# Kernel tuning notes

Hardware: AMD Instinct MI355X
Metric: run time of the kernel (lower is better)

Reference implementation:

```python
import jax, jax.numpy as jnp
import numpy as np
from jax.scipy.special import logsumexp

EXPERT_NUM = 64
MOE_TOPK = 2

def setup_inputs() -> dict:
    key = jax.random.key(0)
    k1, k2 = jax.random.split(key)
    x = jax.random.normal(k1, (4, 4096, 4096), dtype=jnp.float32)
    # nn.Linear(input_size, expert_num).weight has shape [expert_num, input_size]
    W = jax.random.normal(k2, (EXPERT_NUM, 4096), dtype=jnp.float32) * (1.0 / np.sqrt(4096))
    return {"x": x, "W": W}

def reference(x, W):
    # logits: [B, S, E]
    logits = jnp.einsum('bsd,ed->bse', x, W)
    k = min(MOE_TOPK + 1, EXPERT_NUM)  # torch takes topk+1 then slices
    topk_logits, topk_indices = jax.lax.top_k(logits, k)
    topk_logits = topk_logits[..., :MOE_TOPK]     # [B, S, K]
    topk_indices = topk_indices[..., :MOE_TOPK]   # [B, S, K]
    # regularized=True: softmax over the top-k logits in float32
    topk_scores = jax.nn.softmax(topk_logits.astype(jnp.float32), axis=-1).astype(logits.dtype)
    # scatter into zeros; topk indices are unique so one-hot sum == scatter-set
    scores_filtered = jnp.sum(
        jax.nn.one_hot(topk_indices, EXPERT_NUM, dtype=logits.dtype) * topk_scores[..., None],
        axis=-2)  # [B, S, E]
    # router_z loss, per-token [B, S]
    log_z = logsumexp(logits, axis=-1)
    loss = log_z ** 2
    return logits, scores_filtered, loss
```

## Files before the change

kernel.cpp:

```cpp
#include <hip/hip_runtime.h>
#include <math.h>

#define TTOK 16384
#define DD   4096
#define EE   64
#define TM   64
#define BK   64
#define KSL  4
#define KW   (DD / KSL)
#define NCHB (KW / BK)

typedef __attribute__((ext_vector_type(8))) short short8;
typedef __attribute__((ext_vector_type(4))) float f32x4;

static __device__ __forceinline__ unsigned short f2bf(float f) {
    unsigned u = __float_as_uint(f);
    u += 0x7FFFu + ((u >> 16) & 1u);
    return (unsigned short)(u >> 16);
}
static __device__ __forceinline__ float bf2f(unsigned short h) {
    return __uint_as_float(((unsigned)h) << 16);
}
static __device__ __forceinline__ void cvt8(float4 a, float4 b, short8& hi, short8& lo) {
    const float v[8] = {a.x, a.y, a.z, a.w, b.x, b.y, b.z, b.w};
#pragma unroll
    for (int j = 0; j < 8; ++j) {
        const unsigned short h = f2bf(v[j]);
        hi[j] = (short)h;
        lo[j] = (short)f2bf(v[j] - bf2f(h));
    }
}

__global__ void w_convert(const float* __restrict__ W,
                          unsigned short* __restrict__ whi,
                          unsigned short* __restrict__ wlo) {
    const int i = (blockIdx.x * blockDim.x + threadIdx.x) * 4;
    if (i >= EE * DD) return;
    const float4 v = *reinterpret_cast<const float4*>(W + i);
    ushort4 h, l;
    h.x = f2bf(v.x); l.x = f2bf(v.x - bf2f(h.x));
    h.y = f2bf(v.y); l.y = f2bf(v.y - bf2f(h.y));
    h.z = f2bf(v.z); l.z = f2bf(v.z - bf2f(h.z));
    h.w = f2bf(v.w); l.w = f2bf(v.w - bf2f(h.w));
    *reinterpret_cast<ushort4*>(whi + i) = h;
    *reinterpret_cast<ushort4*>(wlo + i) = l;
}

__global__ __launch_bounds__(256, 4)
void gemm_part(const float* __restrict__ x,
               const unsigned short* __restrict__ whi,
               const unsigned short* __restrict__ wlo,
               float* __restrict__ part)
{
    __shared__ unsigned short xh[TM * 64];
    __shared__ unsigned short xl[TM * 64];
    __shared__ unsigned short whs[TM * 64];
    __shared__ unsigned short wls[TM * 64];

    const int tid  = threadIdx.x;
    const int wv   = tid >> 6;
    const int lane = tid & 63;
    const int m    = lane & 15;
    const int q    = lane >> 4;
    const int tile = blockIdx.x & 255;
    const int ks   = blockIdx.x >> 8;
    const int t0   = tile * TM;
    const int k0   = ks * KW;

    const int sr = tid >> 3;
    const int sj = tid & 7;
    const int sp = (sj ^ (sr & 7)) * 8;

    const float* gx0          = x   + (size_t)(t0 + sr) * DD + k0 + sj * 8;
    const float* gx1          = gx0 + (size_t)32 * DD;
    const unsigned short* gh0 = whi + (size_t)sr * DD + k0 + sj * 8;
    const unsigned short* gh1 = gh0 + (size_t)32 * DD;
    const unsigned short* gl0 = wlo + (size_t)sr * DD + k0 + sj * 8;
    const unsigned short* gl1 = gl0 + (size_t)32 * DD;

    unsigned short* const lds_r0 = (unsigned short*)0 + sr * 64 + sp;
    const int o0 = sr * 64 + sp;
    const int o1 = (sr + 32) * 64 + sp;
    (void)lds_r0;

    f32x4 acc[4];
#pragma unroll
    for (int e = 0; e < 4; ++e) acc[e] = (f32x4){0.f, 0.f, 0.f, 0.f};

    float4 fx00 = *reinterpret_cast<const float4*>(gx0);
    float4 fx01 = *reinterpret_cast<const float4*>(gx0 + 4);
    float4 fx10 = *reinterpret_cast<const float4*>(gx1);
    float4 fx11 = *reinterpret_cast<const float4*>(gx1 + 4);
    short8 pwh0 = *reinterpret_cast<const short8*>(gh0);
    short8 pwh1 = *reinterpret_cast<const short8*>(gh1);
    short8 pwl0 = *reinterpret_cast<const short8*>(gl0);
    short8 pwl1 = *reinterpret_cast<const short8*>(gl1);

    const int sa = m & 7;
    const int ra = (16 * wv + m) * 64;

    for (int kc = 0; kc < NCHB; ++kc) {
        __syncthreads();
        {
            short8 h, l;
            cvt8(fx00, fx01, h, l);
            *reinterpret_cast<short8*>(xh + o0) = h;
            *reinterpret_cast<short8*>(xl + o0) = l;
            cvt8(fx10, fx11, h, l);
            *reinterpret_cast<short8*>(xh + o1) = h;
            *reinterpret_cast<short8*>(xl + o1) = l;
            *reinterpret_cast<short8*>(whs + o0) = pwh0;
            *reinterpret_cast<short8*>(whs + o1) = pwh1;
            *reinterpret_cast<short8*>(wls + o0) = pwl0;
            *reinterpret_cast<short8*>(wls + o1) = pwl1;
        }
        __syncthreads();

        if (kc + 1 < NCHB) {
            const int off = (kc + 1) * BK;
            fx00 = *reinterpret_cast<const float4*>(gx0 + off);
            fx01 = *reinterpret_cast<const float4*>(gx0 + off + 4);
            fx10 = *reinterpret_cast<const float4*>(gx1 + off);
            fx11 = *reinterpret_cast<const float4*>(gx1 + off + 4);
            pwh0 = *reinterpret_cast<const short8*>(gh0 + off);
            pwh1 = *reinterpret_cast<const short8*>(gh1 + off);
            pwl0 = *reinterpret_cast<const short8*>(gl0 + off);
            pwl1 = *reinterpret_cast<const short8*>(gl1 + off);
        }

#pragma unroll
        for (int kss = 0; kss < 2; ++kss) {
            const int ca = ((4 * kss + q) ^ sa) * 8;
            const short8 ah = *reinterpret_cast<const short8*>(xh + ra + ca);
            const short8 al = *reinterpret_cast<const short8*>(xl + ra + ca);
#pragma unroll
            for (int e = 0; e < 4; ++e) {
                const int rb = (16 * e + m) * 64;
                const short8 bh = *reinterpret_cast<const short8*>(whs + rb + ca);
                const short8 bl = *reinterpret_cast<const short8*>(wls + rb + ca);
                acc[e] = __builtin_amdgcn_mfma_f32_16x16x32_bf16(ah, bh, acc[e], 0, 0, 0);
                acc[e] = __builtin_amdgcn_mfma_f32_16x16x32_bf16(ah, bl, acc[e], 0, 0, 0);
                acc[e] = __builtin_amdgcn_mfma_f32_16x16x32_bf16(al, bh, acc[e], 0, 0, 0);
            }
        }
    }

    float* pb = part + ((size_t)ks * TTOK + t0 + 16 * wv + 4 * q) * EE + m;
#pragma unroll
    for (int e = 0; e < 4; ++e)
#pragma unroll
        for (int i = 0; i < 4; ++i)
            pb[(size_t)i * EE + 16 * e] = acc[e][i];
}

__global__ __launch_bounds__(256, 4)
void gate_epi(const float* __restrict__ part, float* __restrict__ out)
{
    __shared__ float lg[TM * 68];
    __shared__ float s1a[TM], s2a[TM];
    __shared__ int   i1a[TM], i2a[TM];

    const int tid = threadIdx.x;
    const int t0  = blockIdx.x * TM;
    const int tt  = tid >> 2;
    const int e0  = (tid & 3) * 16;

    const float* pbase = part + (size_t)(t0 + tt) * EE + e0;
    float4 s[4];
#pragma unroll
    for (int j = 0; j < 4; ++j) s[j] = *reinterpret_cast<const float4*>(pbase + 4 * j);
#pragma unroll
    for (int k = 1; k < KSL; ++k) {
        const float* pk = pbase + (size_t)k * TTOK * EE;
#pragma unroll
        for (int j = 0; j < 4; ++j) {
            const float4 r = *reinterpret_cast<const float4*>(pk + 4 * j);
            s[j].x += r.x; s[j].y += r.y; s[j].z += r.z; s[j].w += r.w;
        }
    }
    float* g = out + (size_t)(t0 + tt) * EE + e0;
    float* lrow = lg + tt * 68 + e0;
#pragma unroll
    for (int j = 0; j < 4; ++j) {
        *reinterpret_cast<float4*>(g + 4 * j)    = s[j];
        *reinterpret_cast<float4*>(lrow + 4 * j) = s[j];
    }
    __syncthreads();

    if (tid < TM) {
        const float* row = lg + tid * 68;
        float v1 = -INFINITY, v2 = -INFINITY;
        int   i1 = 0, i2 = 0;
        for (int e = 0; e < EE; ++e) {
            const float v = row[e];
            if (v > v1)      { v2 = v1; i2 = i1; v1 = v; i1 = e; }
            else if (v > v2) { v2 = v;  i2 = e; }
        }
        float sm = 0.f;
        for (int e = 0; e < EE; ++e) sm += expf(row[e] - v1);
        const float logz = v1 + logf(sm);
        out[(size_t)2 * TTOK * EE + t0 + tid] = logz * logz;
        const float e21 = expf(v2 - v1);
        const float rr  = 1.f / (1.f + e21);
        s1a[tid] = rr; s2a[tid] = e21 * rr; i1a[tid] = i1; i2a[tid] = i2;
    }
    __syncthreads();

    float* sc = out + (size_t)TTOK * EE + (size_t)(t0 + tt) * EE + e0;
    const int i1 = i1a[tt], i2 = i2a[tt];
    const float s1 = s1a[tt], s2 = s2a[tt];
#pragma unroll
    for (int j = 0; j < 4; ++j) {
        float vv[4];
#pragma unroll
        for (int c = 0; c < 4; ++c) {
            const int e = e0 + 4 * j + c;
            vv[c] = (e == i1) ? s1 : ((e == i2) ? s2 : 0.f);
        }
        *reinterpret_cast<float4*>(sc + 4 * j) = make_float4(vv[0], vv[1], vv[2], vv[3]);
    }
}

extern "C" void kernel_launch(void* const* d_in, const int* in_sizes, int n_in,
                              void* d_out, int out_size, void* d_ws, size_t ws_size,
                              hipStream_t stream) {
    const float* x = (const float*)d_in[0];
    const float* W = (const float*)d_in[1];
    float* out = (float*)d_out;
    unsigned short* whi = (unsigned short*)d_ws;
    unsigned short* wlo = whi + (size_t)EE * DD;
    float* part = (float*)(wlo + (size_t)EE * DD);

    w_convert<<<dim3((EE * DD / 4 + 255) / 256), dim3(256), 0, stream>>>(W, whi, wlo);
    gemm_part<<<dim3(256 * KSL), dim3(256), 0, stream>>>(x, whi, wlo, part);
    gate_epi<<<dim3(TTOK / TM), dim3(256), 0, stream>>>(part, out);
}
```

Before: 398.1 us.

## Fuse gating GEMM with top-k/softmax epilogue and drop split-K partials

Removes the split-K decomposition and the separate epilogue kernel. Each block now computes 32 tokens across all 64 experts over the full K dimension and runs top-2, softmax and logsumexp in-kernel using 8-lane shuffle reductions. This avoids writing and re-reading the partial-sum buffer and one kernel launch. In exchange, each block reloads and reconverts the full W tile per 32 tokens, so W traffic relative to x grows. Occupancy drops to 512 blocks with launch bounds of 2.

```diff
diff --git a/kernel.cpp b/kernel.cpp
--- a/kernel.cpp
+++ b/kernel.cpp
@@ -4,11 +4,9 @@
 #define TTOK 16384
 #define DD   4096
 #define EE   64
-#define TM   64
+#define TM   32
 #define BK   64
-#define KSL  4
-#define KW   (DD / KSL)
-#define NCHB (KW / BK)
+#define NCH  (DD / BK)
 
 typedef __attribute__((ext_vector_type(8))) short short8;
 typedef __attribute__((ext_vector_type(4))) float f32x4;
@@ -46,82 +44,73 @@
     *reinterpret_cast<ushort4*>(wlo + i) = l;
 }
 
-__global__ __launch_bounds__(256, 4)
-void gemm_part(const float* __restrict__ x,
+__global__ __launch_bounds__(256, 2)
+void moe_fused(const float* __restrict__ x,
                const unsigned short* __restrict__ whi,
                const unsigned short* __restrict__ wlo,
-               float* __restrict__ part)
+               float* __restrict__ out)
 {
     __shared__ unsigned short xh[TM * 64];
     __shared__ unsigned short xl[TM * 64];
-    __shared__ unsigned short whs[TM * 64];
-    __shared__ unsigned short wls[TM * 64];
+    __shared__ unsigned short whs[EE * 64];
+    __shared__ unsigned short wls[EE * 64];
+    __shared__ float lg[TM * 68];
 
     const int tid  = threadIdx.x;
     const int wv   = tid >> 6;
     const int lane = tid & 63;
     const int m    = lane & 15;
     const int q    = lane >> 4;
-    const int tile = blockIdx.x & 255;
-    const int ks   = blockIdx.x >> 8;
-    const int t0   = tile * TM;
-    const int k0   = ks * KW;
+    const int tg   = wv >> 1;
+    const int eh   = wv & 1;
+    const int t0   = blockIdx.x * TM;
 
     const int sr = tid >> 3;
     const int sj = tid & 7;
-    const int sp = (sj ^ (sr & 7)) * 8;
-
-    const float* gx0          = x   + (size_t)(t0 + sr) * DD + k0 + sj * 8;
-    const float* gx1          = gx0 + (size_t)32 * DD;
-    const unsigned short* gh0 = whi + (size_t)sr * DD + k0 + sj * 8;
+    const int sp  = (sj ^ (sr & 7)) * 8;
+    const int xo  = sr * 64 + sp;
+    const int wo0 = xo;
+    const int wo1 = (sr + 32) * 64 + sp;
+
+    const float*          gx  = x   + (size_t)(t0 + sr) * DD + sj * 8;
+    const unsigned short* gh0 = whi + (size_t)sr * DD + sj * 8;
     const unsigned short* gh1 = gh0 + (size_t)32 * DD;
-    const unsigned short* gl0 = wlo + (size_t)sr * DD + k0 + sj * 8;
+    const unsigned short* gl0 = wlo + (size_t)sr * DD + sj * 8;
     const unsigned short* gl1 = gl0 + (size_t)32 * DD;
 
-    unsigned short* const lds_r0 = (unsigned short*)0 + sr * 64 + sp;
-    const int o0 = sr * 64 + sp;
-    const int o1 = (sr + 32) * 64 + sp;
-    (void)lds_r0;
-
-    f32x4 acc[4];
-#pragma unroll
-    for (int e = 0; e < 4; ++e) acc[e] = (f32x4){0.f, 0.f, 0.f, 0.f};
-
-    float4 fx00 = *reinterpret_cast<const float4*>(gx0);
-    float4 fx01 = *reinterpret_cast<const float4*>(gx0 + 4);
-    float4 fx10 = *reinterpret_cast<const float4*>(gx1);
-    float4 fx11 = *reinterpret_cast<const float4*>(gx1 + 4);
+    f32x4 acc0 = (f32x4){0.f, 0.f, 0.f, 0.f};
+    f32x4 acc1 = (f32x4){0.f, 0.f, 0.f, 0.f};
+
+    float4 fx0  = *reinterpret_cast<const float4*>(gx);
+    float4 fx1  = *reinterpret_cast<const float4*>(gx + 4);
     short8 pwh0 = *reinterpret_cast<const short8*>(gh0);
     short8 pwh1 = *reinterpret_cast<const short8*>(gh1);
     short8 pwl0 = *reinterpret_cast<const short8*>(gl0);
     short8 pwl1 = *reinterpret_cast<const short8*>(gl1);
 
-    const int sa = m & 7;
-    const int ra = (16 * wv + m) * 64;
-
-    for (int kc = 0; kc < NCHB; ++kc) {
+    const int sa  = m & 7;
+    const int ra  = (16 * tg + m) * 64;
+    const int rb0 = (32 * eh + m) * 64;
+    const int rb1 = (32 * eh + 16 + m) * 64;
+
+    for (int kc = 0; kc < NCH; ++kc) {
         __syncthreads();
         {
             short8 h, l;
-            cvt8(fx00, fx01, h, l);
-            *reinterpret_cast<short8*>(xh + o0) = h;
-            *reinterpret_cast<short8*>(xl + o0) = l;
-            cvt8(fx10, fx11, h, l);
-            *reinterpret_cast<short8*>(xh + o1) = h;
-            *reinterpret_cast<short8*>(xl + o1) = l;
-            *reinterpret_cast<short8*>(whs + o0) = pwh0;
-            *reinterpret_cast<short8*>(whs + o1) = pwh1;
-            *reinterpret_cast<short8*>(wls + o0) = pwl0;
-            *reinterpret_cast<short8*>(wls + o1) = pwl1;
+            cvt8(fx0, fx1, h, l);
+            *reinterpret_cast<short8*>(xh + xo)   = h;
+            *reinterpret_cast<short8*>(xl + xo)   = l;
+            *reinterpret_cast<short8*>(whs + wo0) = pwh0;
+            *reinterpret_cast<short8*>(whs + wo1) = pwh1;
+            *reinterpret_cast<short8*>(wls + wo0) = pwl0;
+            *reinterpret_cast<short8*>(wls + wo1) = pwl1;
         }
         __syncthreads();
 
-        if (kc + 1 < NCHB) {
+        if (kc + 1 < NCH) {
             const int off = (kc + 1) * BK;
-            fx00 = *reinterpret_cast<const float4*>(gx0 + off);
-            fx01 = *reinterpret_cast<const float4*>(gx0 + off + 4);
-            fx10 = *reinterpret_cast<const float4*>(gx1 + off);
-            fx11 = *reinterpret_cast<const float4*>(gx1 + off + 4);
+            fx0  = *reinterpret_cast<const float4*>(gx + off);
+            fx1  = *reinterpret_cast<const float4*>(gx + off + 4);
             pwh0 = *reinterpret_cast<const short8*>(gh0 + off);
             pwh1 = *reinterpret_cast<const short8*>(gh1 + off);
             pwl0 = *reinterpret_cast<const short8*>(gl0 + off);
@@ -131,94 +120,90 @@
 #pragma unroll
         for (int kss = 0; kss < 2; ++kss) {
             const int ca = ((4 * kss + q) ^ sa) * 8;
-            const short8 ah = *reinterpret_cast<const short8*>(xh + ra + ca);
-            const short8 al = *reinterpret_cast<const short8*>(xl + ra + ca);
-#pragma unroll
-            for (int e = 0; e < 4; ++e) {
-                const int rb = (16 * e + m) * 64;
-                const short8 bh = *reinterpret_cast<const short8*>(whs + rb + ca);
-                const short8 bl = *reinterpret_cast<const short8*>(wls + rb + ca);
-                acc[e] = __builtin_amdgcn_mfma_f32_16x16x32_bf16(ah, bh, acc[e], 0, 0, 0);
-                acc[e] = __builtin_amdgcn_mfma_f32_16x16x32_bf16(ah, bl, acc[e], 0, 0, 0);
-                acc[e] = __builtin_amdgcn_mfma_f32_16x16x32_bf16(al, bh, acc[e], 0, 0, 0);
-            }
-        }
-    }
-
-    float* pb = part + ((size_t)ks * TTOK + t0 + 16 * wv + 4 * q) * EE + m;
-#pragma unroll
-    for (int e = 0; e < 4; ++e)
-#pragma unroll
-        for (int i = 0; i < 4; ++i)
-            pb[(size_t)i * EE + 16 * e] = acc[e][i];
-}
-
-__global__ __launch_bounds__(256, 4)
-void gate_epi(const float* __restrict__ part, float* __restrict__ out)
-{
-    __shared__ float lg[TM * 68];
-    __shared__ float s1a[TM], s2a[TM];
-    __shared__ int   i1a[TM], i2a[TM];
-
-    const int tid = threadIdx.x;
-    const int t0  = blockIdx.x * TM;
-    const int tt  = tid >> 2;
-    const int e0  = (tid & 3) * 16;
-
-    const float* pbase = part + (size_t)(t0 + tt) * EE + e0;
-    float4 s[4];
-#pragma unroll
-    for (int j = 0; j < 4; ++j) s[j] = *reinterpret_cast<const float4*>(pbase + 4 * j);
-#pragma unroll
-    for (int k = 1; k < KSL; ++k) {
-        const float* pk = pbase + (size_t)k * TTOK * EE;
-#pragma unroll
-        for (int j = 0; j < 4; ++j) {
-            const float4 r = *reinterpret_cast<const float4*>(pk + 4 * j);
-            s[j].x += r.x; s[j].y += r.y; s[j].z += r.z; s[j].w += r.w;
-        }
-    }
-    float* g = out + (size_t)(t0 + tt) * EE + e0;
-    float* lrow = lg + tt * 68 + e0;
-#pragma unroll
-    for (int j = 0; j < 4; ++j) {
-        *reinterpret_cast<float4*>(g + 4 * j)    = s[j];
-        *reinterpret_cast<float4*>(lrow + 4 * j) = s[j];
+            const short8 ah  = *reinterpret_cast<const short8*>(xh + ra + ca);
+            const short8 al  = *reinterpret_cast<const short8*>(xl + ra + ca);
+            const short8 bh0 = *reinterpret_cast<const short8*>(whs + rb0 + ca);
+            const short8 bl0 = *reinterpret_cast<const short8*>(wls + rb0 + ca);
+            const short8 bh1 = *reinterpret_cast<const short8*>(whs + rb1 + ca);
+            const short8 bl1 = *reinterpret_cast<const short8*>(wls + rb1 + ca);
+            acc0 = __builtin_amdgcn_mfma_f32_16x16x32_bf16(ah, bh0, acc0, 0, 0, 0);
+            acc0 = __builtin_amdgcn_mfma_f32_16x16x32_bf16(ah, bl0, acc0, 0, 0, 0);
+            acc0 = __builtin_amdgcn_mfma_f32_16x16x32_bf16(al, bh0, acc0, 0, 0, 0);
+            acc1 = __builtin_amdgcn_mfma_f32_16x16x32_bf16(ah, bh1, acc1, 0, 0, 0);
+            acc1 = __builtin_amdgcn_mfma_f32_16x16x32_bf16(ah, bl1, acc1, 0, 0, 0);
+            acc1 = __builtin_amdgcn_mfma_f32_16x16x32_bf16(al, bh1, acc1, 0, 0, 0);
+        }
+    }
+
+    {
+        float* lr = lg + (16 * tg + 4 * q) * 68 + 32 * eh + m;
+#pragma unroll
+        for (int i = 0; i < 4; ++i) {
+            lr[i * 68]      = acc0[i];
+            lr[i * 68 + 16] = acc1[i];
+        }
     }
     __syncthreads();
 
-    if (tid < TM) {
-        const float* row = lg + tid * 68;
-        float v1 = -INFINITY, v2 = -INFINITY;
-        int   i1 = 0, i2 = 0;
-        for (int e = 0; e < EE; ++e) {
-            const float v = row[e];
-            if (v > v1)      { v2 = v1; i2 = i1; v1 = v; i1 = e; }
-            else if (v > v2) { v2 = v;  i2 = e; }
-        }
-        float sm = 0.f;
-        for (int e = 0; e < EE; ++e) sm += expf(row[e] - v1);
-        const float logz = v1 + logf(sm);
-        out[(size_t)2 * TTOK * EE + t0 + tid] = logz * logz;
-        const float e21 = expf(v2 - v1);
-        const float rr  = 1.f / (1.f + e21);
-        s1a[tid] = rr; s2a[tid] = e21 * rr; i1a[tid] = i1; i2a[tid] = i2;
-    }
-    __syncthreads();
-
-    float* sc = out + (size_t)TTOK * EE + (size_t)(t0 + tt) * EE + e0;
-    const int i1 = i1a[tt], i2 = i2a[tt];
-    const float s1 = s1a[tt], s2 = s2a[tt];
-#pragma unroll
-    for (int j = 0; j < 4; ++j) {
-        float vv[4];
-#pragma unroll
-        for (int c = 0; c < 4; ++c) {
-            const int e = e0 + 4 * j + c;
-            vv[c] = (e == i1) ? s1 : ((e == i2) ? s2 : 0.f);
-        }
-        *reinterpret_cast<float4*>(sc + 4 * j) = make_float4(vv[0], vv[1], vv[2], vv[3]);
-    }
+    const int tt = tid >> 3;
+    const int j  = tid & 3 ? (tid & 7) : (tid & 7);
+    const float* row = lg + tt * 68 + (tid & 7) * 8;
+    const int jj = tid & 7;
+    const float4 lv0 = *reinterpret_cast<const float4*>(row);
+    const float4 lv1 = *reinterpret_cast<const float4*>(row + 4);
+    const float r[8] = {lv0.x, lv0.y, lv0.z, lv0.w, lv1.x, lv1.y, lv1.z, lv1.w};
+    (void)j;
+
+    float* gout = out + (size_t)(t0 + tt) * EE + jj * 8;
+    *reinterpret_cast<float4*>(gout)     = lv0;
+    *reinterpret_cast<float4*>(gout + 4) = lv1;
+
+    float v1 = -INFINITY, v2 = -INFINITY;
+    int   i1 = 0, i2 = 0;
+#pragma unroll
+    for (int c = 0; c < 8; ++c) {
+        const int e = jj * 8 + c;
+        const float v = r[c];
+        if (v > v1)      { v2 = v1; i2 = i1; v1 = v; i1 = e; }
+        else if (v > v2) { v2 = v;  i2 = e; }
+    }
+#pragma unroll
+    for (int mk = 1; mk < 8; mk <<= 1) {
+        const float ov1 = __shfl_xor(v1, mk);
+        const int   oi1 = __shfl_xor(i1, mk);
+        const float ov2 = __shfl_xor(v2, mk);
+        const int   oi2 = __shfl_xor(i2, mk);
+        const bool aw = (v1 > ov1) || (v1 == ov1 && i1 < oi1);
+        const float c1v = aw ? v1 : ov1;  const int c1i = aw ? i1 : oi1;
+        const float cav = aw ? v2 : ov2;  const int cai = aw ? i2 : oi2;
+        const float cbv = aw ? ov1 : v1;  const int cbi = aw ? oi1 : i1;
+        const bool bw = (cav > cbv) || (cav == cbv && cai < cbi);
+        v1 = c1v; i1 = c1i;
+        v2 = bw ? cav : cbv;
+        i2 = bw ? cai : cbi;
+    }
+
+    float sm = 0.f;
+#pragma unroll
+    for (int c = 0; c < 8; ++c) sm += expf(r[c] - v1);
+#pragma unroll
+    for (int mk = 1; mk < 8; mk <<= 1) sm += __shfl_xor(sm, mk);
+
+    const float logz = v1 + logf(sm);
+    if (jj == 0) out[(size_t)2 * TTOK * EE + t0 + tt] = logz * logz;
+
+    const float e21 = expf(v2 - v1);
+    const float rr  = 1.f / (1.f + e21);
+    const float s1 = rr, s2 = e21 * rr;
+    float* sc = out + (size_t)TTOK * EE + (size_t)(t0 + tt) * EE + jj * 8;
+    float vv[8];
+#pragma unroll
+    for (int c = 0; c < 8; ++c) {
+        const int e = jj * 8 + c;
+        vv[c] = (e == i1) ? s1 : ((e == i2) ? s2 : 0.f);
+    }
+    *reinterpret_cast<float4*>(sc)     = make_float4(vv[0], vv[1], vv[2], vv[3]);
+    *reinterpret_cast<float4*>(sc + 4) = make_float4(vv[4], vv[5], vv[6], vv[7]);
 }
 
 extern "C" void kernel_launch(void* const* d_in, const int* in_sizes, int n_in,
@@ -229,9 +214,7 @@
     float* out = (float*)d_out;
     unsigned short* whi = (unsigned short*)d_ws;
     unsigned short* wlo = whi + (size_t)EE * DD;
-    float* part = (float*)(wlo + (size_t)EE * DD);
 
     w_convert<<<dim3((EE * DD / 4 + 255) / 256), dim3(256), 0, stream>>>(W, whi, wlo);
-    gemm_part<<<dim3(256 * KSL), dim3(256), 0, stream>>>(x, whi, wlo, part);
-    gate_epi<<<dim3(TTOK / TM), dim3(256), 0, stream>>>(part, out);
-}
+    moe_fused<<<dim3(TTOK / TM), dim3(256), 0, stream>>>(x, whi, wlo, out);
+}
```

After: 383.3 us. 3.7% less time.
